# Kernel optimization log

Hardware: AMD Instinct MI355X
Metric: run time of the kernel (lower is better)

Reference implementation:

```python
import jax, jax.numpy as jnp
import numpy as np

EPS = 1e-8
TEMPERATURE = 1.0  # e0_T, no epoch scaling applied at construction
LABEL_SMOOTH = 0.05


def setup_inputs() -> dict:
    key = jax.random.key(0)
    k1, k2 = jax.random.split(key)
    B, C, H, W = 16, 19, 512, 512
    logits = jax.random.normal(k1, (B, C, H, W), dtype=jnp.float32)
    targets = jax.random.randint(k2, (B, H, W), 0, C, dtype=jnp.int64)
    # confusion matrix initialized as in EMloss.__init__
    off = np.log((LABEL_SMOOTH + EPS) / (C - 1))
    cm = np.full((C, C), off, dtype=np.float32)
    np.fill_diagonal(cm, np.log(1.0 - LABEL_SMOOTH + EPS))
    confusion_matrix = jnp.asarray(cm)
    return {"logits": logits, "targets": targets, "confusion_matrix": confusion_matrix}


def reference(logits, targets, confusion_matrix):
    # temperature softmax over class dim (dim=1); mathematically identical to
    # the original exp(x/T)/sum(exp(x/T)) but numerically stable
    pred = jax.nn.softmax(logits / TEMPERATURE, axis=1)          # [B,C,H,W]
    ncm = jax.nn.softmax(confusion_matrix, axis=1)               # [C,C]
    # pre_p[b,c,h,w] = ncm[c, targets[b,h,w]]  (fused gather over whole batch)
    pre_p = jnp.take(ncm, targets, axis=1)                        # [C,B,H,W]
    pre_p = jnp.transpose(pre_p, (1, 0, 2, 3))                    # [B,C,H,W]
    numel_p = pre_p * pred                                        # [B,C,H,W]
    # q is detached in the original (detach().clone())
    q = jax.lax.stop_gradient(numel_p / numel_p.sum(axis=1, keepdims=True))
    # freeze_confusion=False branch: q * (log(pre_p+eps) + log(pred+eps))
    img_loss = (q * (jnp.log(pre_p + EPS) + jnp.log(pred + EPS))).sum(axis=1)  # [B,H,W]
    per_image = img_loss.mean(axis=(1, 2))                        # [B]
    batch_loss = -per_image.mean()
    return pred, batch_loss
```

## Files before the change

### kernel.cpp

```cpp
#include <hip/hip_runtime.h>

#define EPS 1e-8f

constexpr int B = 16, C = 19, H = 512, W = 512;
constexpr int HW = H * W;
constexpr int NPIX = B * HW;
constexpr long long NPRED = (long long)B * C * HW;


__global__ void ncm_kernel(const float* __restrict__ cm, float* __restrict__ ws) {
    int t = threadIdx.x;
    if (t == 0) ws[768] = 0.0f;
    if (t < C) {
        float row[C];
        float m = -1e30f;
        #pragma unroll
        for (int j = 0; j < C; ++j) { row[j] = cm[t * C + j]; m = fmaxf(m, row[j]); }
        float s = 0.0f;
        #pragma unroll
        for (int j = 0; j < C; ++j) { row[j] = __expf(row[j] - m); s += row[j]; }
        float inv = 1.0f / s;
        #pragma unroll
        for (int j = 0; j < C; ++j) {
            float v = row[j] * inv;
            ws[t * C + j] = v;
            ws[361 + t * C + j] = __logf(v + EPS);
        }
    }
}

__global__ __launch_bounds__(256) void emloss_main(
        const float* __restrict__ logits,
        const int* __restrict__ targets,
        const float* __restrict__ ws,
        float* __restrict__ pred,
        float* __restrict__ loss_acc) {
    __shared__ float s_ncm[C * C];
    __shared__ float s_lpre[C * C];
    for (int i = threadIdx.x; i < C * C; i += blockDim.x) {
        s_ncm[i]  = ws[i];
        s_lpre[i] = ws[361 + i];
    }
    __syncthreads();

    int g = blockIdx.x * blockDim.x + threadIdx.x;
    int pbase = g * 4;
    int b = pbase / HW;
    int r = pbase - b * HW;
    const float* lp = logits + (size_t)b * C * HW + r;
    float*       op = pred   + (size_t)b * C * HW + r;

    float xs[C][4];
    #pragma unroll
    for (int c = 0; c < C; ++c) {
        float4 v = *(const float4*)(lp + (size_t)c * HW);
        xs[c][0] = v.x; xs[c][1] = v.y; xs[c][2] = v.z; xs[c][3] = v.w;
    }
    int4 tv = *(const int4*)(targets + pbase);
    int tt[4] = {tv.x, tv.y, tv.z, tv.w};

    float inv_s[4];
    #pragma unroll
    for (int k = 0; k < 4; ++k) {
        float m = -1e30f;
        #pragma unroll
        for (int c = 0; c < C; ++c) m = fmaxf(m, xs[c][k]);
        float s = 0.0f;
        #pragma unroll
        for (int c = 0; c < C; ++c) {
            float e = __expf(xs[c][k] - m);
            xs[c][k] = e;
            s += e;
        }
        inv_s[k] = 1.0f / s;
    }

    float denom[4] = {0, 0, 0, 0};
    float wsum[4]  = {0, 0, 0, 0};
    #pragma unroll
    for (int c = 0; c < C; ++c) {
        float pk[4];
        #pragma unroll
        for (int k = 0; k < 4; ++k) {
            float p = xs[c][k] * inv_s[k];
            pk[k] = p;
            float nm  = s_ncm[c * C + tt[k]];
            float num = nm * p;
            denom[k] += num;
            wsum[k]  += num * (s_lpre[c * C + tt[k]] + __logf(p + EPS));
        }
        float4 pv = make_float4(pk[0], pk[1], pk[2], pk[3]);
        *(float4*)(op + (size_t)c * HW) = pv;
    }

    float lsum = 0.0f;
    #pragma unroll
    for (int k = 0; k < 4; ++k) lsum += wsum[k] / denom[k];

    #pragma unroll
    for (int off = 32; off > 0; off >>= 1) lsum += __shfl_down(lsum, off);
    if ((threadIdx.x & 63) == 0) atomicAdd(loss_acc, lsum);
}

__global__ void finalize_kernel(const float* __restrict__ acc, float* __restrict__ out) {
    out[0] = -acc[0] / (float)NPIX;
}

extern "C" void kernel_launch(void* const* d_in, const int* in_sizes, int n_in,
                              void* d_out, int out_size, void* d_ws, size_t ws_size,
                              hipStream_t stream) {
    const float* logits  = (const float*)d_in[0];
    const int*   targets = (const int*)d_in[1];
    const float* cm      = (const float*)d_in[2];
    float* out = (float*)d_out;
    float* ws  = (float*)d_ws;

    hipLaunchKernelGGL(ncm_kernel, dim3(1), dim3(64), 0, stream, cm, ws);

    int groups = NPIX / 4;
    int block = 256;
    int grid = groups / block;
    hipLaunchKernelGGL(emloss_main, dim3(grid), dim3(block), 0, stream,
                       logits, targets, ws, out, ws + 768);

    hipLaunchKernelGGL(finalize_kernel, dim3(1), dim3(1), 0, stream,
                       ws + 768, out + NPRED);
}
```

Measured before the change: 616.6 us.

## Replace per-class log with log-softmax identity and process one pixel per thread

Rewrites the loss so log(pred) is expressed as x - max - log(sum), removing one log per class and folding the weighted sum into the exp loop. Switches from four pixels per thread with float4 loads to one pixel per thread with scalar loads, cutting register use. Packs ncm and its log into an interleaved float2 table to halve LDS lookups. Drops the eps inside log(pred), a tiny numerical deviation.

```diff
diff --git a/kernel.cpp b/kernel.cpp
--- a/kernel.cpp
+++ b/kernel.cpp
@@ -20,11 +20,11 @@
         #pragma unroll
         for (int j = 0; j < C; ++j) { row[j] = __expf(row[j] - m); s += row[j]; }
         float inv = 1.0f / s;
+        float2* tab = (float2*)ws;
         #pragma unroll
         for (int j = 0; j < C; ++j) {
             float v = row[j] * inv;
-            ws[t * C + j] = v;
-            ws[361 + t * C + j] = __logf(v + EPS);
+            tab[t * C + j] = make_float2(v, __logf(v + EPS));
         }
     }
 }
@@ -35,67 +35,43 @@
         const float* __restrict__ ws,
         float* __restrict__ pred,
         float* __restrict__ loss_acc) {
-    __shared__ float s_ncm[C * C];
-    __shared__ float s_lpre[C * C];
-    for (int i = threadIdx.x; i < C * C; i += blockDim.x) {
-        s_ncm[i]  = ws[i];
-        s_lpre[i] = ws[361 + i];
-    }
+    __shared__ float2 s_tab[C * C];
+    const float2* tab = (const float2*)ws;
+    for (int i = threadIdx.x; i < C * C; i += blockDim.x) s_tab[i] = tab[i];
     __syncthreads();
 
-    int g = blockIdx.x * blockDim.x + threadIdx.x;
-    int pbase = g * 4;
-    int b = pbase / HW;
-    int r = pbase - b * HW;
+    int p = blockIdx.x * blockDim.x + threadIdx.x;
+    int b = p >> 18;
+    int r = p & (HW - 1);
     const float* lp = logits + (size_t)b * C * HW + r;
     float*       op = pred   + (size_t)b * C * HW + r;
+    int t = targets[p];
 
-    float xs[C][4];
+    float xs[C];
+    #pragma unroll
+    for (int c = 0; c < C; ++c) xs[c] = lp[(size_t)c * HW];
+
+    float m = xs[0];
+    #pragma unroll
+    for (int c = 1; c < C; ++c) m = fmaxf(m, xs[c]);
+
+    float s = 0.0f, denom = 0.0f, A = 0.0f;
     #pragma unroll
     for (int c = 0; c < C; ++c) {
-        float4 v = *(const float4*)(lp + (size_t)c * HW);
-        xs[c][0] = v.x; xs[c][1] = v.y; xs[c][2] = v.z; xs[c][3] = v.w;
-    }
-    int4 tv = *(const int4*)(targets + pbase);
-    int tt[4] = {tv.x, tv.y, tv.z, tv.w};
-
-    float inv_s[4];
-    #pragma unroll
-    for (int k = 0; k < 4; ++k) {
-        float m = -1e30f;
-        #pragma unroll
-        for (int c = 0; c < C; ++c) m = fmaxf(m, xs[c][k]);
-        float s = 0.0f;
-        #pragma unroll
-        for (int c = 0; c < C; ++c) {
-            float e = __expf(xs[c][k] - m);
-            xs[c][k] = e;
-            s += e;
-        }
-        inv_s[k] = 1.0f / s;
+        float e = __expf(xs[c] - m);
+        s += e;
+        float2 nt = s_tab[c * C + t];
+        float ne = nt.x * e;
+        denom += ne;
+        A = fmaf(ne, nt.y + xs[c], A);
+        xs[c] = e;
     }
 
-    float denom[4] = {0, 0, 0, 0};
-    float wsum[4]  = {0, 0, 0, 0};
+    float inv_s = 1.0f / s;
     #pragma unroll
-    for (int c = 0; c < C; ++c) {
-        float pk[4];
-        #pragma unroll
-        for (int k = 0; k < 4; ++k) {
-            float p = xs[c][k] * inv_s[k];
-            pk[k] = p;
-            float nm  = s_ncm[c * C + tt[k]];
-            float num = nm * p;
-            denom[k] += num;
-            wsum[k]  += num * (s_lpre[c * C + tt[k]] + __logf(p + EPS));
-        }
-        float4 pv = make_float4(pk[0], pk[1], pk[2], pk[3]);
-        *(float4*)(op + (size_t)c * HW) = pv;
-    }
+    for (int c = 0; c < C; ++c) op[(size_t)c * HW] = xs[c] * inv_s;
 
-    float lsum = 0.0f;
-    #pragma unroll
-    for (int k = 0; k < 4; ++k) lsum += wsum[k] / denom[k];
+    float lsum = A / denom - (m + __logf(s));
 
     #pragma unroll
     for (int off = 32; off > 0; off >>= 1) lsum += __shfl_down(lsum, off);
@@ -117,9 +93,8 @@
 
     hipLaunchKernelGGL(ncm_kernel, dim3(1), dim3(64), 0, stream, cm, ws);
 
-    int groups = NPIX / 4;
     int block = 256;
-    int grid = groups / block;
+    int grid = NPIX / block;
     hipLaunchKernelGGL(emloss_main, dim3(grid), dim3(block), 0, stream,
                        logits, targets, ws, out, ws + 768);
 
```

Result: slower. 1.219 ms (+97.7%).
